# Kernel tuning notes

Hardware: AMD Instinct MI355X
Metric: run time of the kernel (lower is better)

Reference implementation:

```python
import jax, jax.numpy as jnp
import numpy as np

TOKENS_B, TOKENS_S, N_IN, N_OUT = 8, 2048, 4096, 4096
N8, N4 = 2048, 2048  # channels per format


def setup_inputs() -> dict:
    key = jax.random.key(0)
    k = jax.random.split(key, 7)
    x = jax.random.normal(k[0], (TOKENS_B, TOKENS_S, N_IN), dtype=jnp.float32)
    # int8-format group: values in [-128, 127], per-output-channel scale
    q8 = jax.random.randint(k[1], (N8, N_IN), -128, 128, dtype=jnp.int32)
    s8 = jax.random.uniform(k[2], (N8, 1), dtype=jnp.float32) * 0.01 + 1e-4
    # int4-format group: values in [-8, 7], per-output-channel scale
    q4 = jax.random.randint(k[3], (N4, N_IN), -8, 8, dtype=jnp.int32)
    s4 = jax.random.uniform(k[4], (N4, 1), dtype=jnp.float32) * 0.1 + 1e-4
    # inverse permutation restoring original channel order from [fmt8 | fmt4] concat
    inv_perm = jax.random.permutation(k[5], N_OUT).astype(jnp.int32)
    bias = jax.random.normal(k[6], (N_OUT,), dtype=jnp.float32) * 0.01
    return {"x": x, "q8": q8, "s8": s8, "q4": q4, "s4": s4,
            "inv_perm": inv_perm, "bias": bias}


def reference(x, q8, s8, q4, s4, inv_perm, bias):
    # Per-format dequantize: w = q * scale (per-output-channel scale)
    w8 = q8.astype(jnp.float32) * s8  # [N8, N_IN]
    w4 = q4.astype(jnp.float32) * s4  # [N4, N_IN]
    # Grouped GEMMs, one per format
    y8 = jnp.einsum('bsi,oi->bso', x, w8)  # [B, S, N8]
    y4 = jnp.einsum('bsi,oi->bso', x, w4)  # [B, S, N4]
    # Concat along output channels, then restore original channel order
    y = jnp.concatenate([y8, y4], axis=-1)  # [B, S, N_OUT]
    out = y[..., inv_perm] + bias
    return out
```

## Files before the change

kernel.cpp:

```cpp
#include <hip/hip_runtime.h>


#define M_TOK 16384
#define N_O   4096
#define K_IN  4096
#define N8F   2048
#define NT    (K_IN / 64)

typedef __attribute__((ext_vector_type(4))) int   i32x4;
typedef __attribute__((ext_vector_type(4))) float f32x4;

__device__ __forceinline__ void gl_lds16(const void* g, void* l) {
  __builtin_amdgcn_global_load_lds(
      (const __attribute__((address_space(1))) unsigned int*)g,
      (__attribute__((address_space(3))) unsigned int*)l, 16, 0, 0);
}

__device__ __forceinline__ int clampq(float f) {
  int q = (int)rintf(f);
  return q > 127 ? 127 : (q < -127 ? -127 : q);
}

__global__ void prep_kernel(const float* __restrict__ x,
                            const int4* __restrict__ q8, const float* __restrict__ s8,
                            const int4* __restrict__ q4, const float* __restrict__ s4,
                            const int* __restrict__ inv,
                            char* __restrict__ Wq, float* __restrict__ scale,
                            float* __restrict__ sx, char* __restrict__ xq) {
  __shared__ float red[4];
  const int t = threadIdx.x;
  if (blockIdx.x < N_O) {
    const int j = blockIdx.x;
    const int c = inv[j];
    const int4* src; float s;
    if (c < N8F) { src = q8 + (size_t)c * (K_IN / 4);         s = s8[c]; }
    else         { src = q4 + (size_t)(c - N8F) * (K_IN / 4); s = s4[c - N8F]; }
    if (t == 0) scale[j] = s;
    unsigned dw[4];
#pragma unroll
    for (int i = 0; i < 4; ++i) {
      int4 v = src[t * 4 + i];
      dw[i] = (v.x & 255) | ((v.y & 255) << 8) | ((v.z & 255) << 16)
            | ((unsigned)(v.w & 255) << 24);
    }
    *(uint4*)(Wq + (size_t)j * K_IN + t * 16) = make_uint4(dw[0], dw[1], dw[2], dw[3]);
  } else {
    const int T = blockIdx.x - N_O;
    const float4* xr = (const float4*)(x + (size_t)T * K_IN);
    float4 v[4];
    float m = 0.f;
#pragma unroll
    for (int i = 0; i < 4; ++i) {
      v[i] = xr[t * 4 + i];
      m = fmaxf(m, fmaxf(fmaxf(fabsf(v[i].x), fabsf(v[i].y)),
                         fmaxf(fabsf(v[i].z), fabsf(v[i].w))));
    }
#pragma unroll
    for (int o = 32; o; o >>= 1) m = fmaxf(m, __shfl_xor(m, o));
    if ((t & 63) == 0) red[t >> 6] = m;
    __syncthreads();
    m = fmaxf(fmaxf(red[0], red[1]), fmaxf(red[2], red[3]));
    const float rq = m > 0.f ? 127.f / m : 0.f;
    if (t == 0) sx[T] = m * (1.f / 127.f);
    unsigned dw[4];
#pragma unroll
    for (int i = 0; i < 4; ++i) {
      int a0 = clampq(v[i].x * rq), a1 = clampq(v[i].y * rq);
      int a2 = clampq(v[i].z * rq), a3 = clampq(v[i].w * rq);
      dw[i] = (a0 & 255) | ((a1 & 255) << 8) | ((a2 & 255) << 16)
            | ((unsigned)(a3 & 255) << 24);
    }
    *(uint4*)(xq + (size_t)T * K_IN + t * 16) = make_uint4(dw[0], dw[1], dw[2], dw[3]);
  }
}

__global__ __launch_bounds__(512, 2)
void gemm_i8(const char* __restrict__ xq, const char* __restrict__ Wq,
             const float* __restrict__ sx, const float* __restrict__ scale,
             const float* __restrict__ bias, float* __restrict__ out) {
  __shared__ __align__(16) char sm[65536];
  const int t = threadIdx.x;
  const int w = t >> 6, l = t & 63;
  const int wr = w >> 2, wc = w & 3;
  const int bm = blockIdx.x >> 4, bn = blockIdx.x & 15;
  const int row0 = bm * 256, col0 = bn * 256;

  const int srow = l >> 2;
  const int schunk = ((l & 3) ^ ((l >> 3) & 3)) * 16;
  const char* aG = xq + (size_t)(row0 + w * 16 + srow) * K_IN + schunk;
  const char* bG = Wq + (size_t)(col0 + w * 16 + srow) * K_IN + schunk;
  char* aL0 = sm + w * 1024;
  char* bL0 = sm + 16384 + w * 1024;

  auto stageA = [&](int buf, int kt, int h) {
    gl_lds16(aG + (size_t)h * (128 * K_IN) + kt * 64, aL0 + buf * 32768 + h * 8192);
  };
  auto stageB = [&](int buf, int kt, int h) {
    gl_lds16(bG + (size_t)h * (128 * K_IN) + kt * 64, bL0 + buf * 32768 + h * 8192);
  };

  const int fRoff = (l & 15) * 64 + ((((l >> 4) ^ ((l >> 1) & 3))) << 4);
  const int aOff = wr * 8192 + fRoff;
  const int bOff = 16384 + (wc >> 1) * 8192 + (wc & 1) * 4096 + fRoff;

  i32x4 acc[8][4];
#pragma unroll
  for (int m = 0; m < 8; ++m)
#pragma unroll
    for (int n = 0; n < 4; ++n) acc[m][n] = (i32x4){0, 0, 0, 0};

  stageA(0, 0, 0); stageA(0, 0, 1); stageB(0, 0, 0); stageB(0, 0, 1);
  stageB(1, 1, 0); stageB(1, 1, 1);
  asm volatile("s_waitcnt vmcnt(2)" ::: "memory");
  __builtin_amdgcn_s_barrier();

  i32x4 afr[4], bfr[4];

  for (int kt = 0; kt < NT; ++kt) {
    const int cur = kt & 1;
    const char* smA = sm + cur * 32768 + aOff;
    const char* smB = sm + cur * 32768 + bOff;

#pragma unroll
    for (int n = 0; n < 4; ++n) bfr[n] = *(const i32x4*)(smB + n * 1024);
#pragma unroll
    for (int m = 0; m < 4; ++m) afr[m] = *(const i32x4*)(smA + m * 1024);
    if (kt + 1 < NT) { stageA(cur ^ 1, kt + 1, 0); stageA(cur ^ 1, kt + 1, 1); }
    __builtin_amdgcn_s_barrier();
    asm volatile("s_waitcnt lgkmcnt(0)" ::: "memory");
    __builtin_amdgcn_s_setprio(1);
#pragma unroll
    for (int m = 0; m < 4; ++m)
#pragma unroll
      for (int n = 0; n < 4; ++n)
        acc[m][n] = __builtin_amdgcn_mfma_i32_16x16x64_i8(afr[m], bfr[n],
                                                          acc[m][n], 0, 0, 0);
    __builtin_amdgcn_s_setprio(0);
    __builtin_amdgcn_s_barrier();

#pragma unroll
    for (int m = 0; m < 4; ++m) afr[m] = *(const i32x4*)(smA + (4 + m) * 1024);
    if (kt + 2 < NT) { stageB(cur, kt + 2, 0); stageB(cur, kt + 2, 1); }
    __builtin_amdgcn_s_barrier();
    asm volatile("s_waitcnt lgkmcnt(0)" ::: "memory");
    __builtin_amdgcn_s_setprio(1);
#pragma unroll
    for (int m = 0; m < 4; ++m)
#pragma unroll
      for (int n = 0; n < 4; ++n)
        acc[4 + m][n] = __builtin_amdgcn_mfma_i32_16x16x64_i8(afr[m], bfr[n],
                                                              acc[4 + m][n], 0, 0, 0);
    __builtin_amdgcn_s_setprio(0);
    if (kt + 2 < NT) {
      asm volatile("s_waitcnt vmcnt(2)" ::: "memory");
    } else {
      asm volatile("s_waitcnt vmcnt(0)" ::: "memory");
    }
    __builtin_amdgcn_s_barrier();
  }

  const int orow0 = row0 + wr * 128 + ((l >> 4) << 2);
  const int ocol0 = col0 + wc * 64 + (l & 15);
#pragma unroll
  for (int n = 0; n < 4; ++n) {
    const int col = ocol0 + n * 16;
    const float sc = scale[col];
    const float bi = bias[col];
#pragma unroll
    for (int m = 0; m < 8; ++m) {
      const int r = orow0 + m * 16;
      const float4 sxv = *(const float4*)(sx + r);
      out[(size_t)(r + 0) * N_O + col] = (float)acc[m][n][0] * (sxv.x * sc) + bi;
      out[(size_t)(r + 1) * N_O + col] = (float)acc[m][n][1] * (sxv.y * sc) + bi;
      out[(size_t)(r + 2) * N_O + col] = (float)acc[m][n][2] * (sxv.z * sc) + bi;
      out[(size_t)(r + 3) * N_O + col] = (float)acc[m][n][3] * (sxv.w * sc) + bi;
    }
  }
}

extern "C" void kernel_launch(void* const* d_in, const int* in_sizes, int n_in,
                              void* d_out, int out_size, void* d_ws, size_t ws_size,
                              hipStream_t stream) {
  const float* x    = (const float*)d_in[0];
  const int*   q8   = (const int*)d_in[1];
  const float* s8   = (const float*)d_in[2];
  const int*   q4   = (const int*)d_in[3];
  const float* s4   = (const float*)d_in[4];
  const int*   inv  = (const int*)d_in[5];
  const float* bias = (const float*)d_in[6];
  float* out = (float*)d_out;

  char* ws = (char*)d_ws;
  char*  Wq    = ws;
  float* scale = (float*)(ws + (size_t)N_O * K_IN);
  float* sx    = (float*)(ws + (size_t)N_O * K_IN + 65536);
  char*  xq    = ws + (size_t)N_O * K_IN + 65536 + 65536;

  prep_kernel<<<N_O + M_TOK, 256, 0, stream>>>(x, (const int4*)q8, s8,
                                               (const int4*)q4, s4, inv,
                                               Wq, scale, sx, xq);
  gemm_i8<<<(M_TOK / 256) * (N_O / 256), 512, 0, stream>>>(xq, Wq, sx, scale,
                                                           bias, out);
}
```

Measured before the change: 388.9 us.

## Double K-tile to 128 with four-phase pipelined int8 MFMA loop

Raises the K depth per shared-memory tile from 64 to 128 and doubles the LDS buffer to 128KB, with a new 8-row XOR swizzle. The loop body becomes a four-phase schedule that interleaves A/B global-to-LDS prefetches with eight MFMA groups, and is unrolled by two so the buffer index is a compile-time constant. The goal is fewer loop iterations and less barrier overhead for each unit of MFMA work. The larger LDS footprint likely prevents two blocks from sharing a CU, which can reduce latency hiding.

Result: faster. 380.1 us (-2.3%).

```diff
diff --git a/kernel.cpp b/kernel.cpp
--- a/kernel.cpp
+++ b/kernel.cpp
@@ -5,10 +5,9 @@
 #define N_O   4096
 #define K_IN  4096
 #define N8F   2048
-#define NT    (K_IN / 64)
-
-typedef __attribute__((ext_vector_type(4))) int   i32x4;
-typedef __attribute__((ext_vector_type(4))) float f32x4;
+#define NT    (K_IN / 128)
+
+typedef __attribute__((ext_vector_type(4))) int i32x4;
 
 __device__ __forceinline__ void gl_lds16(const void* g, void* l) {
   __builtin_amdgcn_global_load_lds(
@@ -74,34 +73,115 @@
   }
 }
 
+
+#define CL8(ACCB, AF)                                                                   \
+  __builtin_amdgcn_s_setprio(1);                                                        \
+  _Pragma("unroll") for (int m_ = 0; m_ < 2; ++m_)                                      \
+  _Pragma("unroll") for (int n_ = 0; n_ < 4; ++n_)                                      \
+    acc[(ACCB) + m_][n_] = __builtin_amdgcn_mfma_i32_16x16x64_i8(                       \
+        AF[m_][0], bfr[n_][0], acc[(ACCB) + m_][n_], 0, 0, 0);                          \
+  _Pragma("unroll") for (int m_ = 0; m_ < 2; ++m_)                                      \
+  _Pragma("unroll") for (int n_ = 0; n_ < 4; ++n_)                                      \
+    acc[(ACCB) + m_][n_] = __builtin_amdgcn_mfma_i32_16x16x64_i8(                       \
+        AF[m_][1], bfr[n_][1], acc[(ACCB) + m_][n_], 0, 0, 0);                          \
+  __builtin_amdgcn_s_setprio(0);
+
+#define KTBODY(CUR, kt)                                                                 \
+  {                                                                                     \
+    const char* rA  = (CUR) ? rA1 : rA0;                                                \
+    const char* rAx = (CUR) ? rA1x : rA0x;                                              \
+    const char* rB  = (CUR) ? rB1 : rB0;                                                \
+    const char* rBx = (CUR) ? rB1x : rB0x;                                              \
+    char* aDn = aL0 + ((CUR) ^ 1) * 65536;                  \
+    char* aDc = aL0 + (CUR) * 65536;                         \
+    char* bDc = bL0 + (CUR) * 65536;                         \
+    const int o1 = ((kt) + 1) << 7, o2 = ((kt) + 2) << 7;                               \
+               \
+    _Pragma("unroll") for (int n_ = 0; n_ < 4; ++n_) {                                  \
+      bfr[n_][0] = *(const i32x4*)(rB + n_ * 2048);                                     \
+      bfr[n_][1] = *(const i32x4*)(rBx + n_ * 2048);                                    \
+    }                                                                                   \
+    _Pragma("unroll") for (int m_ = 0; m_ < 2; ++m_) {                                  \
+      afr[m_][0] = *(const i32x4*)(rA + m_ * 2048);                                     \
+      afr[m_][1] = *(const i32x4*)(rAx + m_ * 2048);                                    \
+    }                                                                                   \
+    if ((kt) + 1 < NT) {                                                                \
+      gl_lds16(aG + 524288 + o1, aDn + 16384);                                          \
+      gl_lds16(aG + 524288 + 32768 + o1, aDn + 17408);                                  \
+    }                                                                                   \
+    __builtin_amdgcn_s_barrier();                                                       \
+    asm volatile("s_waitcnt lgkmcnt(0)" ::: "memory");                                  \
+    CL8(0, afr);                                                                        \
+    __builtin_amdgcn_s_barrier();                                                       \
+             \
+    _Pragma("unroll") for (int m_ = 0; m_ < 2; ++m_) {                                  \
+      afr[m_][0] = *(const i32x4*)(rA + (2 + m_) * 2048);                               \
+      afr[m_][1] = *(const i32x4*)(rAx + (2 + m_) * 2048);                              \
+    }                                                                                   \
+    if ((kt) + 2 < NT) {                                                                \
+      gl_lds16(bG + o2, bDc);                                                           \
+      gl_lds16(bG + 32768 + o2, bDc + 1024);                                            \
+    }                                                                                   \
+    __builtin_amdgcn_s_barrier();                                                       \
+    asm volatile("s_waitcnt lgkmcnt(0)" ::: "memory");                                  \
+    CL8(2, afr);                                                                        \
+    __builtin_amdgcn_s_barrier();                                                       \
+                        \
+    _Pragma("unroll") for (int m_ = 0; m_ < 2; ++m_) {                                  \
+      afr[m_][0]  = *(const i32x4*)(rA + (4 + m_) * 2048);                              \
+      afr[m_][1]  = *(const i32x4*)(rAx + (4 + m_) * 2048);                             \
+      afr2[m_][0] = *(const i32x4*)(rA + (6 + m_) * 2048);                              \
+      afr2[m_][1] = *(const i32x4*)(rAx + (6 + m_) * 2048);                             \
+    }                                                                                   \
+    if ((kt) + 2 < NT) {                                                                \
+      gl_lds16(bG + 524288 + o2, bDc + 16384);                                          \
+      gl_lds16(bG + 524288 + 32768 + o2, bDc + 17408);                                  \
+    }                                                                                   \
+    __builtin_amdgcn_s_barrier();                                                       \
+    asm volatile("s_waitcnt lgkmcnt(0)" ::: "memory");                                  \
+    CL8(4, afr);                                                                        \
+    __builtin_amdgcn_s_barrier();                                                       \
+                           \
+    if ((kt) + 2 < NT) {                                                                \
+      gl_lds16(aG + o2, aDc);                                                           \
+      gl_lds16(aG + 32768 + o2, aDc + 1024);                                            \
+      asm volatile("s_waitcnt vmcnt(6)" ::: "memory");                                  \
+    } else {                                                                            \
+      asm volatile("s_waitcnt vmcnt(0)" ::: "memory");                                  \
+    }                                                                                   \
+    __builtin_amdgcn_s_barrier();                                                       \
+    CL8(6, afr2);                                                                       \
+    __builtin_amdgcn_s_barrier();                                                       \
+  }
+
 __global__ __launch_bounds__(512, 2)
 void gemm_i8(const char* __restrict__ xq, const char* __restrict__ Wq,
              const float* __restrict__ sx, const float* __restrict__ scale,
              const float* __restrict__ bias, float* __restrict__ out) {
-  __shared__ __align__(16) char sm[65536];
+  __shared__ __align__(16) char sm[131072];
   const int t = threadIdx.x;
   const int w = t >> 6, l = t & 63;
   const int wr = w >> 2, wc = w & 3;
   const int bm = blockIdx.x >> 4, bn = blockIdx.x & 15;
   const int row0 = bm * 256, col0 = bn * 256;
 
-  const int srow = l >> 2;
-  const int schunk = ((l & 3) ^ ((l >> 3) & 3)) * 16;
+  const int srow = l >> 3;
+  const int schunk = ((l & 7) ^ srow) * 16;
   const char* aG = xq + (size_t)(row0 + w * 16 + srow) * K_IN + schunk;
   const char* bG = Wq + (size_t)(col0 + w * 16 + srow) * K_IN + schunk;
-  char* aL0 = sm + w * 1024;
-  char* bL0 = sm + 16384 + w * 1024;
-
-  auto stageA = [&](int buf, int kt, int h) {
-    gl_lds16(aG + (size_t)h * (128 * K_IN) + kt * 64, aL0 + buf * 32768 + h * 8192);
-  };
-  auto stageB = [&](int buf, int kt, int h) {
-    gl_lds16(bG + (size_t)h * (128 * K_IN) + kt * 64, bL0 + buf * 32768 + h * 8192);
-  };
-
-  const int fRoff = (l & 15) * 64 + ((((l >> 4) ^ ((l >> 1) & 3))) << 4);
-  const int aOff = wr * 8192 + fRoff;
-  const int bOff = 16384 + (wc >> 1) * 8192 + (wc & 1) * 4096 + fRoff;
+  char* aL0 = sm + w * 2048;
+  char* bL0 = sm + 32768 + w * 2048;
+
+  const int lrow128 = (l & 15) * 128;
+  const int cb0 = (((l >> 4) << 4) ^ ((l & 7) << 4));
+  const char* rA0  = sm + wr * 16384 + lrow128 + cb0;
+  const char* rA0x = sm + wr * 16384 + lrow128 + (cb0 ^ 64);
+  const char* rB0  = sm + 32768 + (wc >> 1) * 16384 + (wc & 1) * 8192 + lrow128 + cb0;
+  const char* rB0x = sm + 32768 + (wc >> 1) * 16384 + (wc & 1) * 8192 + lrow128 + (cb0 ^ 64);
+  const char* rA1  = rA0 + 65536;
+  const char* rA1x = rA0x + 65536;
+  const char* rB1  = rB0 + 65536;
+  const char* rB1x = rB0x + 65536;
 
   i32x4 acc[8][4];
 #pragma unroll
@@ -109,54 +189,22 @@
 #pragma unroll
     for (int n = 0; n < 4; ++n) acc[m][n] = (i32x4){0, 0, 0, 0};
 
-  stageA(0, 0, 0); stageA(0, 0, 1); stageB(0, 0, 0); stageB(0, 0, 1);
-  stageB(1, 1, 0); stageB(1, 1, 1);
-  asm volatile("s_waitcnt vmcnt(2)" ::: "memory");
+  gl_lds16(bG, bL0);                 gl_lds16(bG + 32768, bL0 + 1024);
+  gl_lds16(bG + 524288, bL0 + 16384); gl_lds16(bG + 524288 + 32768, bL0 + 17408);
+  gl_lds16(aG, aL0);                 gl_lds16(aG + 32768, aL0 + 1024);
+  gl_lds16(aG + 524288, aL0 + 16384); gl_lds16(aG + 524288 + 32768, aL0 + 17408);
+  gl_lds16(bG + 128, bL0 + 65536);   gl_lds16(bG + 32768 + 128, bL0 + 66560);
+  gl_lds16(bG + 524288 + 128, bL0 + 81920);
+  gl_lds16(bG + 524288 + 32768 + 128, bL0 + 82944);
+  gl_lds16(aG + 128, aL0 + 65536);   gl_lds16(aG + 32768 + 128, aL0 + 66560);
+  asm volatile("s_waitcnt vmcnt(6)" ::: "memory");
   __builtin_amdgcn_s_barrier();
 
-  i32x4 afr[4], bfr[4];
-
-  for (int kt = 0; kt < NT; ++kt) {
-    const int cur = kt & 1;
-    const char* smA = sm + cur * 32768 + aOff;
-    const char* smB = sm + cur * 32768 + bOff;
-
-#pragma unroll
-    for (int n = 0; n < 4; ++n) bfr[n] = *(const i32x4*)(smB + n * 1024);
-#pragma unroll
-    for (int m = 0; m < 4; ++m) afr[m] = *(const i32x4*)(smA + m * 1024);
-    if (kt + 1 < NT) { stageA(cur ^ 1, kt + 1, 0); stageA(cur ^ 1, kt + 1, 1); }
-    __builtin_amdgcn_s_barrier();
-    asm volatile("s_waitcnt lgkmcnt(0)" ::: "memory");
-    __builtin_amdgcn_s_setprio(1);
-#pragma unroll
-    for (int m = 0; m < 4; ++m)
-#pragma unroll
-      for (int n = 0; n < 4; ++n)
-        acc[m][n] = __builtin_amdgcn_mfma_i32_16x16x64_i8(afr[m], bfr[n],
-                                                          acc[m][n], 0, 0, 0);
-    __builtin_amdgcn_s_setprio(0);
-    __builtin_amdgcn_s_barrier();
-
-#pragma unroll
-    for (int m = 0; m < 4; ++m) afr[m] = *(const i32x4*)(smA + (4 + m) * 1024);
-    if (kt + 2 < NT) { stageB(cur, kt + 2, 0); stageB(cur, kt + 2, 1); }
-    __builtin_amdgcn_s_barrier();
-    asm volatile("s_waitcnt lgkmcnt(0)" ::: "memory");
-    __builtin_amdgcn_s_setprio(1);
-#pragma unroll
-    for (int m = 0; m < 4; ++m)
-#pragma unroll
-      for (int n = 0; n < 4; ++n)
-        acc[4 + m][n] = __builtin_amdgcn_mfma_i32_16x16x64_i8(afr[m], bfr[n],
-                                                              acc[4 + m][n], 0, 0, 0);
-    __builtin_amdgcn_s_setprio(0);
-    if (kt + 2 < NT) {
-      asm volatile("s_waitcnt vmcnt(2)" ::: "memory");
-    } else {
-      asm volatile("s_waitcnt vmcnt(0)" ::: "memory");
-    }
-    __builtin_amdgcn_s_barrier();
+  i32x4 bfr[4][2], afr[2][2], afr2[2][2];
+
+  for (int kt = 0; kt < NT; kt += 2) {
+    KTBODY(0, kt);
+    KTBODY(1, kt + 1);
   }
 
   const int orow0 = row0 + wr * 128 + ((l >> 4) << 2);
```

## Double K-tile depth to 128 with simple double-buffered LDS pipeline

Applied to the files above, without the earlier changes.

Raises the K step per iteration from 64 to 128, so the shared-memory footprint grows to 128KB and the swizzle is rewritten for 128-byte rows. The fine-grained split A/B staging, manual waitcnts and setprio are replaced by one stage call per tile and a single __syncthreads per iteration. The goal is fewer barriers and loop iterations per unit of MFMA work. The cost is doubled LDS use, which likely cuts occupancy from the 2 blocks per CU that launch_bounds asks for down to 1. Relying on __syncthreads for the async global-to-LDS loads may also expose load latency.

After: 383.8 us. Within noise of the previous version (-1.3%).

```diff
diff --git a/kernel.cpp b/kernel.cpp
--- a/kernel.cpp
+++ b/kernel.cpp
@@ -5,10 +5,9 @@
 #define N_O   4096
 #define K_IN  4096
 #define N8F   2048
-#define NT    (K_IN / 64)
-
-typedef __attribute__((ext_vector_type(4))) int   i32x4;
-typedef __attribute__((ext_vector_type(4))) float f32x4;
+#define NT    (K_IN / 128)
+
+typedef __attribute__((ext_vector_type(4))) int i32x4;
 
 __device__ __forceinline__ void gl_lds16(const void* g, void* l) {
   __builtin_amdgcn_global_load_lds(
@@ -78,30 +77,40 @@
 void gemm_i8(const char* __restrict__ xq, const char* __restrict__ Wq,
              const float* __restrict__ sx, const float* __restrict__ scale,
              const float* __restrict__ bias, float* __restrict__ out) {
-  __shared__ __align__(16) char sm[65536];
+  __shared__ __align__(16) char sm[131072];
   const int t = threadIdx.x;
   const int w = t >> 6, l = t & 63;
   const int wr = w >> 2, wc = w & 3;
   const int bm = blockIdx.x >> 4, bn = blockIdx.x & 15;
   const int row0 = bm * 256, col0 = bn * 256;
 
-  const int srow = l >> 2;
-  const int schunk = ((l & 3) ^ ((l >> 3) & 3)) * 16;
+  const int srow = l >> 3;
+  const int schunk = ((l & 7) ^ srow) * 16;
   const char* aG = xq + (size_t)(row0 + w * 16 + srow) * K_IN + schunk;
   const char* bG = Wq + (size_t)(col0 + w * 16 + srow) * K_IN + schunk;
-  char* aL0 = sm + w * 1024;
-  char* bL0 = sm + 16384 + w * 1024;
-
-  auto stageA = [&](int buf, int kt, int h) {
-    gl_lds16(aG + (size_t)h * (128 * K_IN) + kt * 64, aL0 + buf * 32768 + h * 8192);
+  char* aL0 = sm + w * 2048;
+  char* bL0 = sm + 32768 + w * 2048;
+
+  auto stage = [&](int buf, int kt) {
+    const int o = kt << 7;
+    char* aD = aL0 + buf * 65536;
+    char* bD = bL0 + buf * 65536;
+    gl_lds16(aG + o, aD);
+    gl_lds16(aG + 32768 + o, aD + 1024);
+    gl_lds16(aG + 524288 + o, aD + 16384);
+    gl_lds16(aG + 524288 + 32768 + o, aD + 17408);
+    gl_lds16(bG + o, bD);
+    gl_lds16(bG + 32768 + o, bD + 1024);
+    gl_lds16(bG + 524288 + o, bD + 16384);
+    gl_lds16(bG + 524288 + 32768 + o, bD + 17408);
   };
-  auto stageB = [&](int buf, int kt, int h) {
-    gl_lds16(bG + (size_t)h * (128 * K_IN) + kt * 64, bL0 + buf * 32768 + h * 8192);
-  };
-
-  const int fRoff = (l & 15) * 64 + ((((l >> 4) ^ ((l >> 1) & 3))) << 4);
-  const int aOff = wr * 8192 + fRoff;
-  const int bOff = 16384 + (wc >> 1) * 8192 + (wc & 1) * 4096 + fRoff;
+
+  const int lrow128 = (l & 15) * 128;
+  const int cb0 = (((l >> 4) << 4) ^ ((l & 7) << 4));
+  const char* rA0  = sm + wr * 16384 + lrow128 + cb0;
+  const char* rA0x = sm + wr * 16384 + lrow128 + (cb0 ^ 64);
+  const char* rB0  = sm + 32768 + (wc >> 1) * 16384 + (wc & 1) * 8192 + lrow128 + cb0;
+  const char* rB0x = sm + 32768 + (wc >> 1) * 16384 + (wc & 1) * 8192 + lrow128 + (cb0 ^ 64);
 
   i32x4 acc[8][4];
 #pragma unroll
@@ -109,54 +118,62 @@
 #pragma unroll
     for (int n = 0; n < 4; ++n) acc[m][n] = (i32x4){0, 0, 0, 0};
 
-  stageA(0, 0, 0); stageA(0, 0, 1); stageB(0, 0, 0); stageB(0, 0, 1);
-  stageB(1, 1, 0); stageB(1, 1, 1);
-  asm volatile("s_waitcnt vmcnt(2)" ::: "memory");
-  __builtin_amdgcn_s_barrier();
-
-  i32x4 afr[4], bfr[4];
-
-  for (int kt = 0; kt < NT; ++kt) {
-    const int cur = kt & 1;
-    const char* smA = sm + cur * 32768 + aOff;
-    const char* smB = sm + cur * 32768 + bOff;
-
-#pragma unroll
-    for (int n = 0; n < 4; ++n) bfr[n] = *(const i32x4*)(smB + n * 1024);
-#pragma unroll
-    for (int m = 0; m < 4; ++m) afr[m] = *(const i32x4*)(smA + m * 1024);
-    if (kt + 1 < NT) { stageA(cur ^ 1, kt + 1, 0); stageA(cur ^ 1, kt + 1, 1); }
-    __builtin_amdgcn_s_barrier();
-    asm volatile("s_waitcnt lgkmcnt(0)" ::: "memory");
-    __builtin_amdgcn_s_setprio(1);
-#pragma unroll
-    for (int m = 0; m < 4; ++m)
-#pragma unroll
-      for (int n = 0; n < 4; ++n)
-        acc[m][n] = __builtin_amdgcn_mfma_i32_16x16x64_i8(afr[m], bfr[n],
-                                                          acc[m][n], 0, 0, 0);
-    __builtin_amdgcn_s_setprio(0);
-    __builtin_amdgcn_s_barrier();
-
-#pragma unroll
-    for (int m = 0; m < 4; ++m) afr[m] = *(const i32x4*)(smA + (4 + m) * 1024);
-    if (kt + 2 < NT) { stageB(cur, kt + 2, 0); stageB(cur, kt + 2, 1); }
-    __builtin_amdgcn_s_barrier();
-    asm volatile("s_waitcnt lgkmcnt(0)" ::: "memory");
-    __builtin_amdgcn_s_setprio(1);
-#pragma unroll
-    for (int m = 0; m < 4; ++m)
-#pragma unroll
-      for (int n = 0; n < 4; ++n)
-        acc[4 + m][n] = __builtin_amdgcn_mfma_i32_16x16x64_i8(afr[m], bfr[n],
-                                                              acc[4 + m][n], 0, 0, 0);
-    __builtin_amdgcn_s_setprio(0);
-    if (kt + 2 < NT) {
-      asm volatile("s_waitcnt vmcnt(2)" ::: "memory");
-    } else {
-      asm volatile("s_waitcnt vmcnt(0)" ::: "memory");
-    }
-    __builtin_amdgcn_s_barrier();
+  stage(0, 0);
+  __syncthreads();
+
+  for (int kt2 = 0; kt2 < NT; kt2 += 2) {
+#pragma unroll
+    for (int half = 0; half < 2; ++half) {
+      const int kt = kt2 + half;
+      const int cur = half;
+      const char* rA  = rA0 + cur * 65536;
+      const char* rAx = rA0x + cur * 65536;
+      const char* rB  = rB0 + cur * 65536;
+      const char* rBx = rB0x + cur * 65536;
+
+      if (kt + 1 < NT) stage(cur ^ 1, kt + 1);
+
+      i32x4 b0[4], b1[4], a0[4], a1[4];
+#pragma unroll
+      for (int n = 0; n < 4; ++n) {
+        b0[n] = *(const i32x4*)(rB + n * 2048);
+        b1[n] = *(const i32x4*)(rBx + n * 2048);
+      }
+#pragma unroll
+      for (int m = 0; m < 4; ++m) a0[m] = *(const i32x4*)(rA + m * 2048);
+#pragma unroll
+      for (int m = 0; m < 4; ++m)
+#pragma unroll
+        for (int n = 0; n < 4; ++n)
+          acc[m][n] = __builtin_amdgcn_mfma_i32_16x16x64_i8(a0[m], b0[n],
+                                                            acc[m][n], 0, 0, 0);
+#pragma unroll
+      for (int m = 0; m < 4; ++m) a1[m] = *(const i32x4*)(rAx + m * 2048);
+#pragma unroll
+      for (int m = 0; m < 4; ++m)
+#pragma unroll
+        for (int n = 0; n < 4; ++n)
+          acc[m][n] = __builtin_amdgcn_mfma_i32_16x16x64_i8(a1[m], b1[n],
+                                                            acc[m][n], 0, 0, 0);
+#pragma unroll
+      for (int m = 0; m < 4; ++m) a0[m] = *(const i32x4*)(rA + (4 + m) * 2048);
+#pragma unroll
+      for (int m = 0; m < 4; ++m)
+#pragma unroll
+        for (int n = 0; n < 4; ++n)
+          acc[4 + m][n] = __builtin_amdgcn_mfma_i32_16x16x64_i8(a0[m], b0[n],
+                                                                acc[4 + m][n], 0, 0, 0);
+#pragma unroll
+      for (int m = 0; m < 4; ++m) a1[m] = *(const i32x4*)(rAx + (4 + m) * 2048);
+#pragma unroll
+      for (int m = 0; m < 4; ++m)
+#pragma unroll
+        for (int n = 0; n < 4; ++n)
+          acc[4 + m][n] = __builtin_amdgcn_mfma_i32_16x16x64_i8(a1[m], b1[n],
+                                                                acc[4 + m][n], 0, 0, 0);
+
+      __syncthreads();
+    }
   }
 
   const int orow0 = row0 + wr * 128 + ((l >> 4) << 2);
```

## Prepack B in MFMA fragment layout and load it directly into registers

Applied to the files above, without the earlier changes.

Splits the prep kernel into an activation quantizer and a weight packer. The packer writes the int8 weights in a fragment-ordered layout so the GEMM can load B straight from global memory into registers, bypassing LDS. Only A now goes through LDS, with a K tile of 128, a new XOR swizzle, and B double-buffered in registers by unrolling the loop two steps at a time. It also adds an XCD-aware tile remap to improve L2 reuse. The cost is higher register pressure, B reads no longer shared through LDS across waves, and one extra kernel launch.

New measurement: 407.5 us. +4.8%, slower.

```diff
diff --git a/kernel.cpp b/kernel.cpp
--- a/kernel.cpp
+++ b/kernel.cpp
@@ -5,10 +5,9 @@
 #define N_O   4096
 #define K_IN  4096
 #define N8F   2048
-#define NT    (K_IN / 64)
-
-typedef __attribute__((ext_vector_type(4))) int   i32x4;
-typedef __attribute__((ext_vector_type(4))) float f32x4;
+#define NT    (K_IN / 128)
+
+typedef __attribute__((ext_vector_type(4))) int i32x4;
 
 __device__ __forceinline__ void gl_lds16(const void* g, void* l) {
   __builtin_amdgcn_global_load_lds(
@@ -21,87 +20,138 @@
   return q > 127 ? 127 : (q < -127 ? -127 : q);
 }
 
-__global__ void prep_kernel(const float* __restrict__ x,
-                            const int4* __restrict__ q8, const float* __restrict__ s8,
-                            const int4* __restrict__ q4, const float* __restrict__ s4,
-                            const int* __restrict__ inv,
-                            char* __restrict__ Wq, float* __restrict__ scale,
-                            float* __restrict__ sx, char* __restrict__ xq) {
+__global__ void prepx_kernel(const float* __restrict__ x,
+                             float* __restrict__ sx, char* __restrict__ xq) {
   __shared__ float red[4];
   const int t = threadIdx.x;
-  if (blockIdx.x < N_O) {
-    const int j = blockIdx.x;
-    const int c = inv[j];
-    const int4* src; float s;
-    if (c < N8F) { src = q8 + (size_t)c * (K_IN / 4);         s = s8[c]; }
-    else         { src = q4 + (size_t)(c - N8F) * (K_IN / 4); s = s4[c - N8F]; }
-    if (t == 0) scale[j] = s;
-    unsigned dw[4];
-#pragma unroll
-    for (int i = 0; i < 4; ++i) {
-      int4 v = src[t * 4 + i];
-      dw[i] = (v.x & 255) | ((v.y & 255) << 8) | ((v.z & 255) << 16)
-            | ((unsigned)(v.w & 255) << 24);
-    }
-    *(uint4*)(Wq + (size_t)j * K_IN + t * 16) = make_uint4(dw[0], dw[1], dw[2], dw[3]);
-  } else {
-    const int T = blockIdx.x - N_O;
-    const float4* xr = (const float4*)(x + (size_t)T * K_IN);
-    float4 v[4];
-    float m = 0.f;
-#pragma unroll
-    for (int i = 0; i < 4; ++i) {
-      v[i] = xr[t * 4 + i];
-      m = fmaxf(m, fmaxf(fmaxf(fabsf(v[i].x), fabsf(v[i].y)),
-                         fmaxf(fabsf(v[i].z), fabsf(v[i].w))));
-    }
-#pragma unroll
-    for (int o = 32; o; o >>= 1) m = fmaxf(m, __shfl_xor(m, o));
-    if ((t & 63) == 0) red[t >> 6] = m;
-    __syncthreads();
-    m = fmaxf(fmaxf(red[0], red[1]), fmaxf(red[2], red[3]));
-    const float rq = m > 0.f ? 127.f / m : 0.f;
-    if (t == 0) sx[T] = m * (1.f / 127.f);
-    unsigned dw[4];
-#pragma unroll
-    for (int i = 0; i < 4; ++i) {
-      int a0 = clampq(v[i].x * rq), a1 = clampq(v[i].y * rq);
-      int a2 = clampq(v[i].z * rq), a3 = clampq(v[i].w * rq);
-      dw[i] = (a0 & 255) | ((a1 & 255) << 8) | ((a2 & 255) << 16)
-            | ((unsigned)(a3 & 255) << 24);
-    }
-    *(uint4*)(xq + (size_t)T * K_IN + t * 16) = make_uint4(dw[0], dw[1], dw[2], dw[3]);
-  }
-}
+  const int T = blockIdx.x;
+  const float4* xr = (const float4*)(x + (size_t)T * K_IN);
+  float4 v[4];
+  float m = 0.f;
+#pragma unroll
+  for (int i = 0; i < 4; ++i) {
+    v[i] = xr[t * 4 + i];
+    m = fmaxf(m, fmaxf(fmaxf(fabsf(v[i].x), fabsf(v[i].y)),
+                       fmaxf(fabsf(v[i].z), fabsf(v[i].w))));
+  }
+#pragma unroll
+  for (int o = 32; o; o >>= 1) m = fmaxf(m, __shfl_xor(m, o));
+  if ((t & 63) == 0) red[t >> 6] = m;
+  __syncthreads();
+  m = fmaxf(fmaxf(red[0], red[1]), fmaxf(red[2], red[3]));
+  const float rq = m > 0.f ? 127.f / m : 0.f;
+  if (t == 0) sx[T] = m * (1.f / 127.f);
+  unsigned dw[4];
+#pragma unroll
+  for (int i = 0; i < 4; ++i) {
+    int a0 = clampq(v[i].x * rq), a1 = clampq(v[i].y * rq);
+    int a2 = clampq(v[i].z * rq), a3 = clampq(v[i].w * rq);
+    dw[i] = (a0 & 255) | ((a1 & 255) << 8) | ((a2 & 255) << 16)
+          | ((unsigned)(a3 & 255) << 24);
+  }
+  *(uint4*)(xq + (size_t)T * K_IN + t * 16) = make_uint4(dw[0], dw[1], dw[2], dw[3]);
+}
+
+__global__ void packb_kernel(const int4* __restrict__ q8, const float* __restrict__ s8,
+                             const int4* __restrict__ q4, const float* __restrict__ s4,
+                             const int* __restrict__ inv,
+                             char* __restrict__ Bf, float* __restrict__ scale) {
+  const int j = blockIdx.x;
+  const int t = threadIdx.x;
+  const int c = inv[j];
+  const int4* src; float s;
+  if (c < N8F) { src = q8 + (size_t)c * (K_IN / 4);         s = s8[c]; }
+  else         { src = q4 + (size_t)(c - N8F) * (K_IN / 4); s = s4[c - N8F]; }
+  if (t == 0) scale[j] = s;
+  unsigned dw[4];
+#pragma unroll
+  for (int i = 0; i < 4; ++i) {
+    int4 v = src[t * 4 + i];
+    dw[i] = (v.x & 255) | ((v.y & 255) << 8) | ((v.z & 255) << 16)
+          | ((unsigned)(v.w & 255) << 24);
+  }
+  const int bn = j >> 8, wcq = (j >> 6) & 3, n = (j >> 4) & 3, lr = j & 15;
+  const int kt = t >> 3, kk = (t >> 2) & 1, lane = ((t & 3) << 4) | lr;
+  char* dst = Bf + (((size_t)bn * 32 + kt) << 15) + wcq * 8192 + kk * 4096 +
+              n * 1024 + lane * 16;
+  *(uint4*)dst = make_uint4(dw[0], dw[1], dw[2], dw[3]);
+}
+
+#define TILEBODY(CUR, kt, BCUR, BNXT)                                                  \
+  {                                                                                    \
+    if ((kt) + 1 < NT) {                                                               \
+      const int o = ((kt) + 1) << 7;                                                   \
+      char* aD = aL0 + ((CUR) ^ 1) * 32768;                                            \
+      gl_lds16(aG + o, aD);                                                            \
+      gl_lds16(aG + 32768 + o, aD + 1024);                                             \
+      gl_lds16(aG + 524288 + o, aD + 16384);                                           \
+      gl_lds16(aG + 524288 + 32768 + o, aD + 17408);                                   \
+      __builtin_amdgcn_sched_barrier(0);          \
+      const char* bp = bBase + (size_t)((kt) + 1) * 32768;                             \
+      _Pragma("unroll") for (int i = 0; i < 8; ++i)                                    \
+        BNXT[i] = *(const i32x4*)(bp + ((i >> 2) << 12) + ((i & 3) << 10));            \
+    }                                                                                  \
+    const char* rA  = rA0 + (CUR) * 32768;                                             \
+    const char* rAx = rA0x + (CUR) * 32768;                                            \
+    i32x4 a0[4], a1[4];                                                                \
+    _Pragma("unroll") for (int m_ = 0; m_ < 4; ++m_)                                   \
+      a0[m_] = *(const i32x4*)(rA + m_ * 2048);                                        \
+    _Pragma("unroll") for (int m_ = 0; m_ < 4; ++m_)                                   \
+    _Pragma("unroll") for (int n_ = 0; n_ < 4; ++n_)                                   \
+      acc[m_][n_] = __builtin_amdgcn_mfma_i32_16x16x64_i8(a0[m_], BCUR[n_],            \
+                                                          acc[m_][n_], 0, 0, 0);       \
+    _Pragma("unroll") for (int m_ = 0; m_ < 4; ++m_)                                   \
+      a1[m_] = *(const i32x4*)(rAx + m_ * 2048);                                       \
+    _Pragma("unroll") for (int m_ = 0; m_ < 4; ++m_)                                   \
+    _Pragma("unroll") for (int n_ = 0; n_ < 4; ++n_)                                   \
+      acc[m_][n_] = __builtin_amdgcn_mfma_i32_16x16x64_i8(a1[m_], BCUR[4 + n_],        \
+                                                          acc[m_][n_], 0, 0, 0);       \
+    _Pragma("unroll") for (int m_ = 0; m_ < 4; ++m_)                                   \
+      a0[m_] = *(const i32x4*)(rA + (4 + m_) * 2048);                                  \
+    _Pragma("unroll") for (int m_ = 0; m_ < 4; ++m_)                                   \
+    _Pragma("unroll") for (int n_ = 0; n_ < 4; ++n_)                                   \
+      acc[4 + m_][n_] = __builtin_amdgcn_mfma_i32_16x16x64_i8(a0[m_], BCUR[n_],        \
+                                                              acc[4 + m_][n_], 0, 0, 0); \
+    _Pragma("unroll") for (int m_ = 0; m_ < 4; ++m_)                                   \
+      a1[m_] = *(const i32x4*)(rAx + (4 + m_) * 2048);                                 \
+    _Pragma("unroll") for (int m_ = 0; m_ < 4; ++m_)                                   \
+    _Pragma("unroll") for (int n_ = 0; n_ < 4; ++n_)                                   \
+      acc[4 + m_][n_] = __builtin_amdgcn_mfma_i32_16x16x64_i8(a1[m_], BCUR[4 + n_],    \
+                                                              acc[4 + m_][n_], 0, 0, 0); \
+    if ((kt) + 1 < NT) {                                                               \
+      asm volatile("s_waitcnt lgkmcnt(0)" ::: "memory");                               \
+      asm volatile("s_waitcnt vmcnt(8)" ::: "memory");        \
+      __builtin_amdgcn_sched_barrier(0);                                               \
+      __builtin_amdgcn_s_barrier();                                                    \
+    }                                                                                  \
+  }
 
 __global__ __launch_bounds__(512, 2)
-void gemm_i8(const char* __restrict__ xq, const char* __restrict__ Wq,
+void gemm_i8(const char* __restrict__ xq, const char* __restrict__ Bf,
              const float* __restrict__ sx, const float* __restrict__ scale,
              const float* __restrict__ bias, float* __restrict__ out) {
   __shared__ __align__(16) char sm[65536];
   const int t = threadIdx.x;
   const int w = t >> 6, l = t & 63;
   const int wr = w >> 2, wc = w & 3;
-  const int bm = blockIdx.x >> 4, bn = blockIdx.x & 15;
-  const int row0 = bm * 256, col0 = bn * 256;
-
-  const int srow = l >> 2;
-  const int schunk = ((l & 3) ^ ((l >> 3) & 3)) * 16;
+  const int wg = blockIdx.x;
+  const int xcd = wg & 7, local_ = wg >> 3;
+  const int sub = local_ >> 5, pos = local_ & 31;
+  const int bm = (xcd << 3) | (pos >> 2);
+  const int bn = (sub << 2) | (pos & 3);
+  const int row0 = bm * 256;
+
+  const int srow = l >> 3;
+  const int schunk = ((l & 7) ^ srow) * 16;
   const char* aG = xq + (size_t)(row0 + w * 16 + srow) * K_IN + schunk;
-  const char* bG = Wq + (size_t)(col0 + w * 16 + srow) * K_IN + schunk;
-  char* aL0 = sm + w * 1024;
-  char* bL0 = sm + 16384 + w * 1024;
-
-  auto stageA = [&](int buf, int kt, int h) {
-    gl_lds16(aG + (size_t)h * (128 * K_IN) + kt * 64, aL0 + buf * 32768 + h * 8192);
-  };
-  auto stageB = [&](int buf, int kt, int h) {
-    gl_lds16(bG + (size_t)h * (128 * K_IN) + kt * 64, bL0 + buf * 32768 + h * 8192);
-  };
-
-  const int fRoff = (l & 15) * 64 + ((((l >> 4) ^ ((l >> 1) & 3))) << 4);
-  const int aOff = wr * 8192 + fRoff;
-  const int bOff = 16384 + (wc >> 1) * 8192 + (wc & 1) * 4096 + fRoff;
+  char* aL0 = sm + w * 2048;
+
+  const int lrow128 = (l & 15) * 128;
+  const int cb0 = (((l >> 4) << 4) ^ ((l & 7) << 4));
+  const char* rA0  = sm + wr * 16384 + lrow128 + cb0;
+  const char* rA0x = sm + wr * 16384 + lrow128 + (cb0 ^ 64);
+
+  const char* bBase = Bf + ((size_t)bn << 20) + wc * 8192 + l * 16;
 
   i32x4 acc[8][4];
 #pragma unroll
@@ -109,58 +159,27 @@
 #pragma unroll
     for (int n = 0; n < 4; ++n) acc[m][n] = (i32x4){0, 0, 0, 0};
 
-  stageA(0, 0, 0); stageA(0, 0, 1); stageB(0, 0, 0); stageB(0, 0, 1);
-  stageB(1, 1, 0); stageB(1, 1, 1);
-  asm volatile("s_waitcnt vmcnt(2)" ::: "memory");
+  i32x4 bP[8], bQ[8];
+
+  gl_lds16(aG, aL0);
+  gl_lds16(aG + 32768, aL0 + 1024);
+  gl_lds16(aG + 524288, aL0 + 16384);
+  gl_lds16(aG + 524288 + 32768, aL0 + 17408);
+  __builtin_amdgcn_sched_barrier(0);
+#pragma unroll
+  for (int i = 0; i < 8; ++i)
+    bP[i] = *(const i32x4*)(bBase + ((i >> 2) << 12) + ((i & 3) << 10));
+  asm volatile("s_waitcnt vmcnt(8)" ::: "memory");
+  __builtin_amdgcn_sched_barrier(0);
   __builtin_amdgcn_s_barrier();
 
-  i32x4 afr[4], bfr[4];
-
-  for (int kt = 0; kt < NT; ++kt) {
-    const int cur = kt & 1;
-    const char* smA = sm + cur * 32768 + aOff;
-    const char* smB = sm + cur * 32768 + bOff;
-
-#pragma unroll
-    for (int n = 0; n < 4; ++n) bfr[n] = *(const i32x4*)(smB + n * 1024);
-#pragma unroll
-    for (int m = 0; m < 4; ++m) afr[m] = *(const i32x4*)(smA + m * 1024);
-    if (kt + 1 < NT) { stageA(cur ^ 1, kt + 1, 0); stageA(cur ^ 1, kt + 1, 1); }
-    __builtin_amdgcn_s_barrier();
-    asm volatile("s_waitcnt lgkmcnt(0)" ::: "memory");
-    __builtin_amdgcn_s_setprio(1);
-#pragma unroll
-    for (int m = 0; m < 4; ++m)
-#pragma unroll
-      for (int n = 0; n < 4; ++n)
-        acc[m][n] = __builtin_amdgcn_mfma_i32_16x16x64_i8(afr[m], bfr[n],
-                                                          acc[m][n], 0, 0, 0);
-    __builtin_amdgcn_s_setprio(0);
-    __builtin_amdgcn_s_barrier();
-
-#pragma unroll
-    for (int m = 0; m < 4; ++m) afr[m] = *(const i32x4*)(smA + (4 + m) * 1024);
-    if (kt + 2 < NT) { stageB(cur, kt + 2, 0); stageB(cur, kt + 2, 1); }
-    __builtin_amdgcn_s_barrier();
-    asm volatile("s_waitcnt lgkmcnt(0)" ::: "memory");
-    __builtin_amdgcn_s_setprio(1);
-#pragma unroll
-    for (int m = 0; m < 4; ++m)
-#pragma unroll
-      for (int n = 0; n < 4; ++n)
-        acc[4 + m][n] = __builtin_amdgcn_mfma_i32_16x16x64_i8(afr[m], bfr[n],
-                                                              acc[4 + m][n], 0, 0, 0);
-    __builtin_amdgcn_s_setprio(0);
-    if (kt + 2 < NT) {
-      asm volatile("s_waitcnt vmcnt(2)" ::: "memory");
-    } else {
-      asm volatile("s_waitcnt vmcnt(0)" ::: "memory");
-    }
-    __builtin_amdgcn_s_barrier();
+  for (int kt = 0; kt < NT; kt += 2) {
+    TILEBODY(0, kt, bP, bQ);
+    TILEBODY(1, kt + 1, bQ, bP);
   }
 
   const int orow0 = row0 + wr * 128 + ((l >> 4) << 2);
-  const int ocol0 = col0 + wc * 64 + (l & 15);
+  const int ocol0 = bn * 256 + wc * 64 + (l & 15);
 #pragma unroll
   for (int n = 0; n < 4; ++n) {
     const int col = ocol0 + n * 16;
@@ -191,14 +210,14 @@
   float* out = (float*)d_out;
 
   char* ws = (char*)d_ws;
-  char*  Wq    = ws;
+  char*  Bf    = ws;
   float* scale = (float*)(ws + (size_t)N_O * K_IN);
   float* sx    = (float*)(ws + (size_t)N_O * K_IN + 65536);
   char*  xq    = ws + (size_t)N_O * K_IN + 65536 + 65536;
 
-  prep_kernel<<<N_O + M_TOK, 256, 0, stream>>>(x, (const int4*)q8, s8,
-                                               (const int4*)q4, s4, inv,
-                                               Wq, scale, sx, xq);
-  gemm_i8<<<(M_TOK / 256) * (N_O / 256), 512, 0, stream>>>(xq, Wq, sx, scale,
+  prepx_kernel<<<M_TOK, 256, 0, stream>>>(x, sx, xq);
+  packb_kernel<<<N_O, 256, 0, stream>>>((const int4*)q8, s8, (const int4*)q4, s4,
+                                        inv, Bf, scale);
+  gemm_i8<<<(M_TOK / 256) * (N_O / 256), 512, 0, stream>>>(xq, Bf, sx, scale,
                                                            bias, out);
 }
```
